# Optimization experiments

Hardware: AMD Instinct MI355X
Metric: run time of the kernel (lower is better)

Reference implementation:

```python
import jax, jax.numpy as jnp
import numpy as np

N_NODES = 100000
N_EDGES = 3200000
IN_CH = 128
HID = 32


def setup_inputs() -> dict:
    key = jax.random.key(0)
    k1, k2, k3, k4 = jax.random.split(key, 4)
    x = jax.random.normal(k1, (N_NODES, IN_CH), dtype=jnp.float32)
    edge_index = jax.random.randint(k2, (2, N_EDGES), 0, N_NODES, dtype=jnp.int64)
    # Glorot-style scale for weights
    W1 = jax.random.normal(k3, (IN_CH, HID), dtype=jnp.float32) * (1.0 / np.sqrt(IN_CH))
    b1 = jnp.zeros((HID,), dtype=jnp.float32)
    W2 = jax.random.normal(k4, (HID, HID), dtype=jnp.float32) * (1.0 / np.sqrt(HID))
    b2 = jnp.zeros((HID,), dtype=jnp.float32)
    return {"x": x, "edge_index": edge_index, "W1": W1, "b1": b1, "W2": W2, "b2": b2}


def _gcn_conv(x, src, dst, norm, W, b, n_nodes):
    # PyG GCNConv: h = x @ W, then symmetric-normalized scatter-add, then + bias
    h = x @ W                                   # [N, out]
    msg = h[src] * norm[:, None]                # gather + per-edge scale
    out = jax.ops.segment_sum(msg, dst, num_segments=n_nodes)  # scatter-add
    return out + b


def reference(x, edge_index, W1, b1, W2, b2):
    n = x.shape[0]
    loop = jnp.arange(n, dtype=edge_index.dtype)
    # add self-loops (PyG default add_self_loops=True)
    src = jnp.concatenate([edge_index[0], loop])
    dst = jnp.concatenate([edge_index[1], loop])
    # symmetric normalization deg^-1/2 on destination-side in-degree (incl. self-loops)
    deg = jax.ops.segment_sum(jnp.ones_like(dst, dtype=x.dtype), dst, num_segments=n)
    dinv = jnp.where(deg > 0, jax.lax.rsqrt(deg), 0.0)
    norm = dinv[src] * dinv[dst]                # [E + N]
    h = _gcn_conv(x, src, dst, norm, W1, b1, n)
    h = jax.nn.relu(h)
    out = _gcn_conv(h, src, dst, norm, W2, b2, n)
    return out
```

## Files before the change

kernel.cpp:

```cpp
#include <hip/hip_runtime.h>
#include <hip/hip_bf16.h>

#define N_NODES 100000
#define N_EDGES 3200000
#define IN_CH   128
#define HID     32
#define NB      1024
#define NPB     98
#define CAP     4096
#define CHUNK   4096
#define EPT     8
#define ACC_LD  33
#define NPASS   8
#define OCTN    12500u
#define FXS     1048576.0f
#define FXI     (1.0f/1048576.0f)
#define NTILE   6250
#define TPW     2

__device__ __forceinline__ unsigned int pack_bf16x2(float a, float b) {
    unsigned int ua = __float_as_uint(a);
    unsigned int ub = __float_as_uint(b);
    ua = (ua + 0x7FFFu + ((ua >> 16) & 1u)) >> 16;
    ub = (ub + 0x7FFFu + ((ub >> 16) & 1u)) >> 16;
    return (ua & 0xFFFFu) | (ub << 16);
}
__device__ __forceinline__ float bf_lo(unsigned int v) { return __uint_as_float(v << 16); }
__device__ __forceinline__ float bf_hi(unsigned int v) { return __uint_as_float(v & 0xFFFF0000u); }
__device__ __forceinline__ int   f2fx(float f)         { return (int)(f * FXS); }
__device__ __forceinline__ float hif(float f) {
    return __uint_as_float(__float_as_uint(f) & 0xFFFF0000u);
}
__device__ __forceinline__ unsigned int tpack(float a, float b) {
    return (__float_as_uint(a) >> 16) | (__float_as_uint(b) & 0xFFFF0000u);
}
__device__ __forceinline__ unsigned short bf16_rne(float f) {
    unsigned int u = __float_as_uint(f);
    return (unsigned short)((u + 0x7FFFu + ((u >> 16) & 1u)) >> 16);
}

typedef short bf16x8 __attribute__((ext_vector_type(8)));
typedef float f32x4  __attribute__((ext_vector_type(4)));
union frag_u { bf16x8 f; unsigned int u[4]; };

__global__ __launch_bounds__(256) void detect_idx(const int* __restrict__ ei,
                                                  int* __restrict__ flag) {
    __shared__ int nz;
    if (threadIdx.x == 0) nz = 0;
    __syncthreads();
    if (ei[2 * threadIdx.x + 1] != 0) atomicAdd(&nz, 1);
    __syncthreads();
    if (threadIdx.x == 0) flag[0] = (nz == 0) ? 1 : 0;
}

__device__ __forceinline__ int edge_at(const int* __restrict__ ei, int idx64,
                                       size_t pos) {
    if (idx64) return (int)((const long long*)ei)[pos];
    return ei[pos];
}

__global__ __launch_bounds__(256) void bcur_init(int* __restrict__ bcur) {
    int b = blockIdx.x * 256 + threadIdx.x;
    if (b < NB) bcur[b] = b * CAP;
}

__global__ __launch_bounds__(512) void bucket_scatter5(
    const int* __restrict__ ei,
    const int* __restrict__ flag,
    int* __restrict__ bcur,
    unsigned int* __restrict__ ebuf) {
    __shared__ int cnt[NB];
    __shared__ int loff[NB];
    __shared__ int dlt[NB];
    __shared__ int tmp[512];
    __shared__ unsigned int   sbuf[CHUNK];
    __shared__ unsigned short sbb[CHUNK];

    int t = threadIdx.x;
    for (int j = t; j < NB; j += 512) cnt[j] = 0;
    __syncthreads();

    int e0 = blockIdx.x * CHUNK;
    int nE = N_EDGES - e0; if (nE > CHUNK) nE = CHUNK;
    int idx64 = flag[0];

    unsigned int rs[EPT], rd[EPT];
#pragma unroll
    for (int j = 0; j < EPT; ++j) {
        int i = t + j * 512;
        if (i < nE) {
            rs[j] = (unsigned int)edge_at(ei, idx64, (size_t)(e0 + i));
            rd[j] = (unsigned int)edge_at(ei, idx64, (size_t)N_EDGES + e0 + i);
        }
    }

#pragma unroll
    for (int j = 0; j < EPT; ++j) {
        int i = t + j * 512;
        if (i < nE) atomicAdd(&cnt[rd[j] / NPB], 1);
    }
    __syncthreads();

    int c0 = cnt[2 * t], c1 = cnt[2 * t + 1];
    int s = c0 + c1;
    tmp[t] = s;
    __syncthreads();
    for (int off = 1; off < 512; off <<= 1) {
        int x = 0;
        if (t >= off) x = tmp[t - off];
        __syncthreads();
        if (t >= off) tmp[t] += x;
        __syncthreads();
    }
    int base = tmp[t] - s;
    loff[2 * t]     = base;
    loff[2 * t + 1] = base + c0;
    __syncthreads();

    for (int j = t; j < NB; j += 512) {
        int c = cnt[j];
        int gb = (c > 0) ? atomicAdd(&bcur[j], c) : 0;
        dlt[j] = gb - loff[j];
        cnt[j] = 0;
    }
    __syncthreads();

#pragma unroll
    for (int j = 0; j < EPT; ++j) {
        int i = t + j * 512;
        if (i < nE) {
            unsigned int b = rd[j] / NPB;
            int pos = loff[b] + atomicAdd(&cnt[b], 1);
            sbuf[pos] = (rs[j] << 8) | (rd[j] - b * NPB);
            sbb[pos]  = (unsigned short)b;
        }
    }
    __syncthreads();

    for (int i = t; i < nE; i += 512)
        ebuf[dlt[sbb[i]] + i] = sbuf[i];
}

__global__ __launch_bounds__(512) void finalize_csr(
    const int* __restrict__ bcur,
    unsigned int* __restrict__ ebuf,
    float* __restrict__ dinv,
    int* __restrict__ octp) {
    __shared__ unsigned int lbuf[CAP];
    __shared__ unsigned int sbuf[CAP];
    __shared__ int lhist[NPB];
    __shared__ int oh[8];
    __shared__ int obase[9];
    __shared__ int ocur[8];
    int b = blockIdx.x, t = threadIdx.x;
    int n0 = b * NPB;
    int nn = N_NODES - n0; if (nn > NPB) nn = NPB; if (nn < 0) nn = 0;
    int cnt = bcur[b] - b * CAP;
    unsigned int* reg = ebuf + (size_t)b * CAP;

    for (int j = t; j < NPB; j += 512) lhist[j] = 0;
    if (t < 8) oh[t] = 0;
    __syncthreads();

    for (int i = t; i < cnt; i += 512) {
        unsigned int e = reg[i];
        lbuf[i] = e;
        atomicAdd(&lhist[e & 255u], 1);
        atomicAdd(&oh[(e >> 8) / OCTN], 1);
    }
    __syncthreads();

    for (int j = t; j < nn; j += 512)
        dinv[n0 + j] = rsqrtf((float)(lhist[j] + 1));

    if (t == 0) {
        obase[0] = 0;
        for (int p = 0; p < 8; ++p) {
            obase[p + 1] = obase[p] + oh[p];
            ocur[p] = obase[p];
        }
    }
    __syncthreads();

    for (int i = t; i < cnt; i += 512) {
        unsigned int e = lbuf[i];
        int p = (int)((e >> 8) / OCTN);
        int pos = atomicAdd(&ocur[p], 1);
        sbuf[pos] = e;
    }
    __syncthreads();

    for (int i = t; i < cnt; i += 512)
        reg[i] = sbuf[i];
    if (t < 9) octp[b * 9 + t] = obase[t];
}

__global__ __launch_bounds__(256) void gemm1_mfma(
    const float* __restrict__ x,
    const float* __restrict__ W1,
    const float* __restrict__ dinv,
    unsigned short* __restrict__ h1u) {
    int wv   = blockIdx.x * 4 + (threadIdx.x >> 6);
    int lane = threadIdx.x & 63;
    int lq   = lane & 15;
    int kh   = lane >> 4;

    frag_u bh[2][4], bl[2][4];
#pragma unroll
    for (int t = 0; t < 2; ++t) {
#pragma unroll
        for (int s = 0; s < 4; ++s) {
            int ch = t * 16 + lq;
            int k0 = s * 32 + kh * 8;
            float w[8], wh[8];
#pragma unroll
            for (int i = 0; i < 8; ++i) {
                w[i]  = W1[(k0 + i) * HID + ch];
                wh[i] = hif(w[i]);
            }
#pragma unroll
            for (int j = 0; j < 4; ++j) {
                bh[t][s].u[j] = tpack(wh[2 * j], wh[2 * j + 1]);
                bl[t][s].u[j] = tpack(w[2 * j] - wh[2 * j],
                                      w[2 * j + 1] - wh[2 * j + 1]);
            }
        }
    }

#pragma unroll 1
    for (int it = 0; it < TPW; ++it) {
        int tile = wv * TPW + it;
        if (tile >= NTILE) return;
        int n0 = tile * 16;
        const float* xr = x + (size_t)(n0 + lq) * IN_CH;

        f32x4 acc0 = {0.f, 0.f, 0.f, 0.f};
        f32x4 acc1 = {0.f, 0.f, 0.f, 0.f};
#pragma unroll
        for (int s = 0; s < 4; ++s) {
            int k0 = s * 32 + kh * 8;
            float4 v0 = *reinterpret_cast<const float4*>(xr + k0);
            float4 v1 = *reinterpret_cast<const float4*>(xr + k0 + 4);
            frag_u ah, al;
            ah.u[0] = tpack(v0.x, v0.y);
            ah.u[1] = tpack(v0.z, v0.w);
            ah.u[2] = tpack(v1.x, v1.y);
            ah.u[3] = tpack(v1.z, v1.w);
            al.u[0] = tpack(v0.x - hif(v0.x), v0.y - hif(v0.y));
            al.u[1] = tpack(v0.z - hif(v0.z), v0.w - hif(v0.w));
            al.u[2] = tpack(v1.x - hif(v1.x), v1.y - hif(v1.y));
            al.u[3] = tpack(v1.z - hif(v1.z), v1.w - hif(v1.w));

            acc0 = __builtin_amdgcn_mfma_f32_16x16x32_bf16(ah.f, bh[0][s].f, acc0, 0, 0, 0);
            acc0 = __builtin_amdgcn_mfma_f32_16x16x32_bf16(al.f, bh[0][s].f, acc0, 0, 0, 0);
            acc0 = __builtin_amdgcn_mfma_f32_16x16x32_bf16(ah.f, bl[0][s].f, acc0, 0, 0, 0);
            acc1 = __builtin_amdgcn_mfma_f32_16x16x32_bf16(ah.f, bh[1][s].f, acc1, 0, 0, 0);
            acc1 = __builtin_amdgcn_mfma_f32_16x16x32_bf16(al.f, bh[1][s].f, acc1, 0, 0, 0);
            acc1 = __builtin_amdgcn_mfma_f32_16x16x32_bf16(ah.f, bl[1][s].f, acc1, 0, 0, 0);
        }

#pragma unroll
        for (int j = 0; j < 4; ++j) {
            int node = n0 + kh * 4 + j;
            float dn = dinv[node];
            unsigned short* dst = h1u + (size_t)node * 32 + lq;
            dst[0]  = bf16_rne(acc0[j] * dn);
            dst[16] = bf16_rne(acc1[j] * dn);
        }
    }
}

__device__ __forceinline__ uint4 row_q(const unsigned int* __restrict__ hb,
                                       unsigned int s, int q4) {
    return *reinterpret_cast<const uint4*>(hb + (size_t)s * 16 + q4);
}

__device__ __forceinline__ void fx_scatter8(int* acc, unsigned int e,
                                            int co, uint4 v) {
    int* a = acc + (int)(e & 255u) * ACC_LD + co;
    atomicAdd(&a[0], f2fx(bf_lo(v.x))); atomicAdd(&a[1], f2fx(bf_hi(v.x)));
    atomicAdd(&a[2], f2fx(bf_lo(v.y))); atomicAdd(&a[3], f2fx(bf_hi(v.y)));
    atomicAdd(&a[4], f2fx(bf_lo(v.z))); atomicAdd(&a[5], f2fx(bf_hi(v.z)));
    atomicAdd(&a[6], f2fx(bf_lo(v.w))); atomicAdd(&a[7], f2fx(bf_hi(v.w)));
}

__global__ __launch_bounds__(512, 8) void agg1_srt(
    const int* __restrict__ bcur,
    const unsigned int* __restrict__ ebuf,
    const int* __restrict__ octp,
    const unsigned int* __restrict__ h1b,
    const float* __restrict__ dinv,
    const float* __restrict__ b1,
    const float* __restrict__ W2,
    unsigned int* __restrict__ h3b) {
    __shared__ int acc[NPB * ACC_LD];
    __shared__ float w2s[HID * HID];
    __shared__ float b1s[HID];
    int b = blockIdx.x, t = threadIdx.x;
    int n0 = b * NPB;
    int nn = N_NODES - n0; if (nn > NPB) nn = NPB; if (nn < 0) nn = 0;
    const unsigned int* reg = ebuf + (size_t)b * CAP;

    for (int i = t; i < HID * HID; i += 512) w2s[i] = W2[i];
    if (t < HID) b1s[t] = b1[t];

    for (int u = t; u < nn * 4; u += 512) {
        int n = u >> 2, q = u & 3;
        uint4 sv = *reinterpret_cast<const uint4*>(h1b + (size_t)(n0 + n) * 16 + 4 * q);
        int* a = &acc[n * ACC_LD + 8 * q];
        a[0] = f2fx(bf_lo(sv.x)); a[1] = f2fx(bf_hi(sv.x));
        a[2] = f2fx(bf_lo(sv.y)); a[3] = f2fx(bf_hi(sv.y));
        a[4] = f2fx(bf_lo(sv.z)); a[5] = f2fx(bf_hi(sv.z));
        a[6] = f2fx(bf_lo(sv.w)); a[7] = f2fx(bf_hi(sv.w));
    }
    __syncthreads();

    int q4 = (t & 3) * 4;
    int co = (t & 3) * 8;
#pragma unroll 1
    for (int p = 0; p < NPASS; ++p) {
        int o1 = octp[b * 9 + p + 1];
        int i  = octp[b * 9 + p] + (t >> 2);
        for (; i + 128 < o1; i += 256) {
            unsigned int e0 = reg[i];
            unsigned int e1 = reg[i + 128];
            uint4 v0 = row_q(h1b, e0 >> 8, q4);
            uint4 v1 = row_q(h1b, e1 >> 8, q4);
            fx_scatter8(acc, e0, co, v0);
            fx_scatter8(acc, e1, co, v1);
        }
        if (i < o1) {
            unsigned int e = reg[i];
            uint4 v = row_q(h1b, e >> 8, q4);
            fx_scatter8(acc, e, co, v);
        }
    }
    __syncthreads();

    float* h2s = (float*)acc;
    for (int u = t; u < nn * HID; u += 512) {
        int n = u >> 5, j = u & 31;
        float v = (float)acc[n * ACC_LD + j] * FXI * dinv[n0 + n] + b1s[j];
        h2s[n * ACC_LD + j] = v > 0.f ? v : 0.f;
    }
    __syncthreads();

    for (int u = t; u < nn * 4; u += 512) {
        int n = u >> 2, qq = u & 3;
        const float* h2 = &h2s[n * ACC_LD];
        float a2[8];
#pragma unroll
        for (int k = 0; k < 8; ++k) a2[k] = 0.f;
#pragma unroll
        for (int j = 0; j < HID; ++j) {
            float hj = h2[j];
            const float* wr = &w2s[j * HID + 8 * qq];
#pragma unroll
            for (int k = 0; k < 8; ++k) a2[k] += hj * wr[k];
        }
        float dn = dinv[n0 + n];
        unsigned int* dst = h3b + (size_t)(n0 + n) * 16 + 4 * qq;
        *reinterpret_cast<uint4*>(dst) = make_uint4(
            pack_bf16x2(a2[0] * dn, a2[1] * dn),
            pack_bf16x2(a2[2] * dn, a2[3] * dn),
            pack_bf16x2(a2[4] * dn, a2[5] * dn),
            pack_bf16x2(a2[6] * dn, a2[7] * dn));
    }
}

__global__ __launch_bounds__(512, 8) void agg2_srt(
    const int* __restrict__ bcur,
    const unsigned int* __restrict__ ebuf,
    const int* __restrict__ octp,
    const unsigned int* __restrict__ h3b,
    const float* __restrict__ dinv,
    const float* __restrict__ b2,
    float* __restrict__ out) {
    __shared__ int acc[NPB * ACC_LD];
    __shared__ float b2s[HID];
    int b = blockIdx.x, t = threadIdx.x;
    int n0 = b * NPB;
    int nn = N_NODES - n0; if (nn > NPB) nn = NPB; if (nn < 0) nn = 0;
    const unsigned int* reg = ebuf + (size_t)b * CAP;

    if (t < HID) b2s[t] = b2[t];

    for (int u = t; u < nn * 4; u += 512) {
        int n = u >> 2, q = u & 3;
        uint4 sv = *reinterpret_cast<const uint4*>(h3b + (size_t)(n0 + n) * 16 + 4 * q);
        int* a = &acc[n * ACC_LD + 8 * q];
        a[0] = f2fx(bf_lo(sv.x)); a[1] = f2fx(bf_hi(sv.x));
        a[2] = f2fx(bf_lo(sv.y)); a[3] = f2fx(bf_hi(sv.y));
        a[4] = f2fx(bf_lo(sv.z)); a[5] = f2fx(bf_hi(sv.z));
        a[6] = f2fx(bf_lo(sv.w)); a[7] = f2fx(bf_hi(sv.w));
    }
    __syncthreads();

    int q4 = (t & 3) * 4;
    int co = (t & 3) * 8;
#pragma unroll 1
    for (int p = 0; p < NPASS; ++p) {
        int o1 = octp[b * 9 + p + 1];
        int i  = octp[b * 9 + p] + (t >> 2);
        for (; i + 128 < o1; i += 256) {
            unsigned int e0 = reg[i];
            unsigned int e1 = reg[i + 128];
            uint4 v0 = row_q(h3b, e0 >> 8, q4);
            uint4 v1 = row_q(h3b, e1 >> 8, q4);
            fx_scatter8(acc, e0, co, v0);
            fx_scatter8(acc, e1, co, v1);
        }
        if (i < o1) {
            unsigned int e = reg[i];
            uint4 v = row_q(h3b, e >> 8, q4);
            fx_scatter8(acc, e, co, v);
        }
    }
    __syncthreads();

    for (int u = t; u < nn * 4; u += 512) {
        int n = u >> 2, qq = u & 3;
        float dn = dinv[n0 + n];
        const int* a = &acc[n * ACC_LD + 8 * qq];
        const float* bb = &b2s[8 * qq];
        float4 o1v, o2v;
        o1v.x = (float)a[0] * FXI * dn + bb[0];
        o1v.y = (float)a[1] * FXI * dn + bb[1];
        o1v.z = (float)a[2] * FXI * dn + bb[2];
        o1v.w = (float)a[3] * FXI * dn + bb[3];
        o2v.x = (float)a[4] * FXI * dn + bb[4];
        o2v.y = (float)a[5] * FXI * dn + bb[5];
        o2v.z = (float)a[6] * FXI * dn + bb[6];
        o2v.w = (float)a[7] * FXI * dn + bb[7];
        float* op = out + (size_t)(n0 + n) * 32 + 8 * qq;
        *reinterpret_cast<float4*>(op)     = o1v;
        *reinterpret_cast<float4*>(op + 4) = o2v;
    }
}

extern "C" void kernel_launch(void* const* d_in, const int* in_sizes, int n_in,
                              void* d_out, int out_size, void* d_ws, size_t ws_size,
                              hipStream_t stream) {
    const float* x  = (const float*)d_in[0];
    const int*   ei = (const int*)d_in[1];
    const float* W1 = (const float*)d_in[2];
    const float* b1 = (const float*)d_in[3];
    const float* W2 = (const float*)d_in[4];
    const float* b2 = (const float*)d_in[5];
    float* out = (float*)d_out;

    int*          flag = (int*)d_ws;
    int*          bcur = flag + 64;
    int*          octp = bcur + NB;
    float*        dinv = (float*)(octp + NB * 9);
    unsigned int* ebuf = (unsigned int*)(dinv + N_NODES);
    unsigned int* h1b  = ebuf + (size_t)NB * CAP;
    unsigned int* h3b  = h1b + (size_t)N_NODES * 16;

    const int chunkBlocks = (N_EDGES + CHUNK - 1) / CHUNK;
    const int g1Blocks    = (NTILE + 4 * TPW - 1) / (4 * TPW);

    detect_idx<<<1, 256, 0, stream>>>(ei, flag);

    bcur_init<<<(NB + 255) / 256, 256, 0, stream>>>(bcur);
    bucket_scatter5<<<chunkBlocks, 512, 0, stream>>>(ei, flag, bcur, ebuf);
    finalize_csr<<<NB, 512, 0, stream>>>(bcur, ebuf, dinv, octp);

    gemm1_mfma<<<g1Blocks, 256, 0, stream>>>(x, W1, dinv,
                                             (unsigned short*)h1b);
    agg1_srt<<<NB, 512, 0, stream>>>(bcur, ebuf, octp, h1b, dinv, b1, W2, h3b);

    agg2_srt<<<NB, 512, 0, stream>>>(bcur, ebuf, octp, h3b, dinv, b2, out);
}
```

Baseline: 218.3 us.

## Flatten aggregation loops, merge init kernels, enlarge scatter chunks, rotate bucket atomics

Several changes at once. The aggregation kernels drop the per-octant pass structure and octp table and walk each bucket's edges in one flat loop unrolled by four. bcur initialization is folded into the detect kernel, which removes one launch. The bucket scatter doubles its chunk size and edges per thread and rotates the order of its global atomics per block to spread contention. finalize_csr moves to 256 threads. It still sorts edges by source octant, so locality is kept while the per-pass loop overhead goes away; the larger scatter chunks raise LDS use and lower the block count.

```diff
diff --git a/kernel.cpp b/kernel.cpp
--- a/kernel.cpp
+++ b/kernel.cpp
@@ -8,10 +8,9 @@
 #define NB      1024
 #define NPB     98
 #define CAP     4096
-#define CHUNK   4096
-#define EPT     8
+#define CHUNK   8192
+#define EPT     16
 #define ACC_LD  33
-#define NPASS   8
 #define OCTN    12500u
 #define FXS     1048576.0f
 #define FXI     (1.0f/1048576.0f)
@@ -43,9 +42,11 @@
 typedef float f32x4  __attribute__((ext_vector_type(4)));
 union frag_u { bf16x8 f; unsigned int u[4]; };
 
-__global__ __launch_bounds__(256) void detect_idx(const int* __restrict__ ei,
-                                                  int* __restrict__ flag) {
+__global__ __launch_bounds__(256) void detect_init(const int* __restrict__ ei,
+                                                   int* __restrict__ flag,
+                                                   int* __restrict__ bcur) {
     __shared__ int nz;
+    for (int j = threadIdx.x; j < NB; j += 256) bcur[j] = j * CAP;
     if (threadIdx.x == 0) nz = 0;
     __syncthreads();
     if (ei[2 * threadIdx.x + 1] != 0) atomicAdd(&nz, 1);
@@ -59,12 +60,7 @@
     return ei[pos];
 }
 
-__global__ __launch_bounds__(256) void bcur_init(int* __restrict__ bcur) {
-    int b = blockIdx.x * 256 + threadIdx.x;
-    if (b < NB) bcur[b] = b * CAP;
-}
-
-__global__ __launch_bounds__(512) void bucket_scatter5(
+__global__ __launch_bounds__(512) void scatter7(
     const int* __restrict__ ei,
     const int* __restrict__ flag,
     int* __restrict__ bcur,
@@ -117,7 +113,9 @@
     loff[2 * t + 1] = base + c0;
     __syncthreads();
 
-    for (int j = t; j < NB; j += 512) {
+    int rot = (blockIdx.x * 211) & (NB - 1);
+    for (int jj = t; jj < NB; jj += 512) {
+        int j = (jj + rot) & (NB - 1);
         int c = cnt[j];
         int gb = (c > 0) ? atomicAdd(&bcur[j], c) : 0;
         dlt[j] = gb - loff[j];
@@ -141,16 +139,15 @@
         ebuf[dlt[sbb[i]] + i] = sbuf[i];
 }
 
-__global__ __launch_bounds__(512) void finalize_csr(
+__global__ __launch_bounds__(256) void finalize_csr(
     const int* __restrict__ bcur,
     unsigned int* __restrict__ ebuf,
-    float* __restrict__ dinv,
-    int* __restrict__ octp) {
+    float* __restrict__ dinv) {
     __shared__ unsigned int lbuf[CAP];
     __shared__ unsigned int sbuf[CAP];
     __shared__ int lhist[NPB];
     __shared__ int oh[8];
-    __shared__ int obase[9];
+    __shared__ int obase[8];
     __shared__ int ocur[8];
     int b = blockIdx.x, t = threadIdx.x;
     int n0 = b * NPB;
@@ -158,11 +155,11 @@
     int cnt = bcur[b] - b * CAP;
     unsigned int* reg = ebuf + (size_t)b * CAP;
 
-    for (int j = t; j < NPB; j += 512) lhist[j] = 0;
+    for (int j = t; j < NPB; j += 256) lhist[j] = 0;
     if (t < 8) oh[t] = 0;
     __syncthreads();
 
-    for (int i = t; i < cnt; i += 512) {
+    for (int i = t; i < cnt; i += 256) {
         unsigned int e = reg[i];
         lbuf[i] = e;
         atomicAdd(&lhist[e & 255u], 1);
@@ -170,19 +167,18 @@
     }
     __syncthreads();
 
-    for (int j = t; j < nn; j += 512)
+    for (int j = t; j < nn; j += 256)
         dinv[n0 + j] = rsqrtf((float)(lhist[j] + 1));
 
     if (t == 0) {
-        obase[0] = 0;
+        int run = 0;
         for (int p = 0; p < 8; ++p) {
-            obase[p + 1] = obase[p] + oh[p];
-            ocur[p] = obase[p];
-        }
-    }
-    __syncthreads();
-
-    for (int i = t; i < cnt; i += 512) {
+            obase[p] = run; ocur[p] = run; run += oh[p];
+        }
+    }
+    __syncthreads();
+
+    for (int i = t; i < cnt; i += 256) {
         unsigned int e = lbuf[i];
         int p = (int)((e >> 8) / OCTN);
         int pos = atomicAdd(&ocur[p], 1);
@@ -190,9 +186,8 @@
     }
     __syncthreads();
 
-    for (int i = t; i < cnt; i += 512)
+    for (int i = t; i < cnt; i += 256)
         reg[i] = sbuf[i];
-    if (t < 9) octp[b * 9 + t] = obase[t];
 }
 
 __global__ __launch_bounds__(256) void gemm1_mfma(
@@ -284,10 +279,9 @@
     atomicAdd(&a[6], f2fx(bf_lo(v.w))); atomicAdd(&a[7], f2fx(bf_hi(v.w)));
 }
 
-__global__ __launch_bounds__(512, 8) void agg1_srt(
+__global__ __launch_bounds__(512, 8) void agg1_flat(
     const int* __restrict__ bcur,
     const unsigned int* __restrict__ ebuf,
-    const int* __restrict__ octp,
     const unsigned int* __restrict__ h1b,
     const float* __restrict__ dinv,
     const float* __restrict__ b1,
@@ -299,6 +293,7 @@
     int b = blockIdx.x, t = threadIdx.x;
     int n0 = b * NPB;
     int nn = N_NODES - n0; if (nn > NPB) nn = NPB; if (nn < 0) nn = 0;
+    int cnt = bcur[b] - b * CAP;
     const unsigned int* reg = ebuf + (size_t)b * CAP;
 
     for (int i = t; i < HID * HID; i += 512) w2s[i] = W2[i];
@@ -317,23 +312,25 @@
 
     int q4 = (t & 3) * 4;
     int co = (t & 3) * 8;
-#pragma unroll 1
-    for (int p = 0; p < NPASS; ++p) {
-        int o1 = octp[b * 9 + p + 1];
-        int i  = octp[b * 9 + p] + (t >> 2);
-        for (; i + 128 < o1; i += 256) {
-            unsigned int e0 = reg[i];
-            unsigned int e1 = reg[i + 128];
-            uint4 v0 = row_q(h1b, e0 >> 8, q4);
-            uint4 v1 = row_q(h1b, e1 >> 8, q4);
-            fx_scatter8(acc, e0, co, v0);
-            fx_scatter8(acc, e1, co, v1);
-        }
-        if (i < o1) {
-            unsigned int e = reg[i];
-            uint4 v = row_q(h1b, e >> 8, q4);
-            fx_scatter8(acc, e, co, v);
-        }
+    int i  = t >> 2;
+    for (; i + 384 < cnt; i += 512) {
+        unsigned int e0 = reg[i];
+        unsigned int e1 = reg[i + 128];
+        unsigned int e2 = reg[i + 256];
+        unsigned int e3 = reg[i + 384];
+        uint4 v0 = row_q(h1b, e0 >> 8, q4);
+        uint4 v1 = row_q(h1b, e1 >> 8, q4);
+        uint4 v2 = row_q(h1b, e2 >> 8, q4);
+        uint4 v3 = row_q(h1b, e3 >> 8, q4);
+        fx_scatter8(acc, e0, co, v0);
+        fx_scatter8(acc, e1, co, v1);
+        fx_scatter8(acc, e2, co, v2);
+        fx_scatter8(acc, e3, co, v3);
+    }
+    for (; i < cnt; i += 128) {
+        unsigned int e = reg[i];
+        uint4 v = row_q(h1b, e >> 8, q4);
+        fx_scatter8(acc, e, co, v);
     }
     __syncthreads();
 
@@ -368,10 +365,9 @@
     }
 }
 
-__global__ __launch_bounds__(512, 8) void agg2_srt(
+__global__ __launch_bounds__(512, 8) void agg2_flat(
     const int* __restrict__ bcur,
     const unsigned int* __restrict__ ebuf,
-    const int* __restrict__ octp,
     const unsigned int* __restrict__ h3b,
     const float* __restrict__ dinv,
     const float* __restrict__ b2,
@@ -381,6 +377,7 @@
     int b = blockIdx.x, t = threadIdx.x;
     int n0 = b * NPB;
     int nn = N_NODES - n0; if (nn > NPB) nn = NPB; if (nn < 0) nn = 0;
+    int cnt = bcur[b] - b * CAP;
     const unsigned int* reg = ebuf + (size_t)b * CAP;
 
     if (t < HID) b2s[t] = b2[t];
@@ -398,23 +395,25 @@
 
     int q4 = (t & 3) * 4;
     int co = (t & 3) * 8;
-#pragma unroll 1
-    for (int p = 0; p < NPASS; ++p) {
-        int o1 = octp[b * 9 + p + 1];
-        int i  = octp[b * 9 + p] + (t >> 2);
-        for (; i + 128 < o1; i += 256) {
-            unsigned int e0 = reg[i];
-            unsigned int e1 = reg[i + 128];
-            uint4 v0 = row_q(h3b, e0 >> 8, q4);
-            uint4 v1 = row_q(h3b, e1 >> 8, q4);
-            fx_scatter8(acc, e0, co, v0);
-            fx_scatter8(acc, e1, co, v1);
-        }
-        if (i < o1) {
-            unsigned int e = reg[i];
-            uint4 v = row_q(h3b, e >> 8, q4);
-            fx_scatter8(acc, e, co, v);
-        }
+    int i  = t >> 2;
+    for (; i + 384 < cnt; i += 512) {
+        unsigned int e0 = reg[i];
+        unsigned int e1 = reg[i + 128];
+        unsigned int e2 = reg[i + 256];
+        unsigned int e3 = reg[i + 384];
+        uint4 v0 = row_q(h3b, e0 >> 8, q4);
+        uint4 v1 = row_q(h3b, e1 >> 8, q4);
+        uint4 v2 = row_q(h3b, e2 >> 8, q4);
+        uint4 v3 = row_q(h3b, e3 >> 8, q4);
+        fx_scatter8(acc, e0, co, v0);
+        fx_scatter8(acc, e1, co, v1);
+        fx_scatter8(acc, e2, co, v2);
+        fx_scatter8(acc, e3, co, v3);
+    }
+    for (; i < cnt; i += 128) {
+        unsigned int e = reg[i];
+        uint4 v = row_q(h3b, e >> 8, q4);
+        fx_scatter8(acc, e, co, v);
     }
     __syncthreads();
 
@@ -451,8 +450,7 @@
 
     int*          flag = (int*)d_ws;
     int*          bcur = flag + 64;
-    int*          octp = bcur + NB;
-    float*        dinv = (float*)(octp + NB * 9);
+    float*        dinv = (float*)(bcur + NB);
     unsigned int* ebuf = (unsigned int*)(dinv + N_NODES);
     unsigned int* h1b  = ebuf + (size_t)NB * CAP;
     unsigned int* h3b  = h1b + (size_t)N_NODES * 16;
@@ -460,15 +458,14 @@
     const int chunkBlocks = (N_EDGES + CHUNK - 1) / CHUNK;
     const int g1Blocks    = (NTILE + 4 * TPW - 1) / (4 * TPW);
 
-    detect_idx<<<1, 256, 0, stream>>>(ei, flag);
-
-    bcur_init<<<(NB + 255) / 256, 256, 0, stream>>>(bcur);
-    bucket_scatter5<<<chunkBlocks, 512, 0, stream>>>(ei, flag, bcur, ebuf);
-    finalize_csr<<<NB, 512, 0, stream>>>(bcur, ebuf, dinv, octp);
+    detect_init<<<1, 256, 0, stream>>>(ei, flag, bcur);
+
+    scatter7<<<chunkBlocks, 512, 0, stream>>>(ei, flag, bcur, ebuf);
+    finalize_csr<<<NB, 256, 0, stream>>>(bcur, ebuf, dinv);
 
     gemm1_mfma<<<g1Blocks, 256, 0, stream>>>(x, W1, dinv,
                                              (unsigned short*)h1b);
-    agg1_srt<<<NB, 512, 0, stream>>>(bcur, ebuf, octp, h1b, dinv, b1, W2, h3b);
-
-    agg2_srt<<<NB, 512, 0, stream>>>(bcur, ebuf, octp, h3b, dinv, b2, out);
-}
+    agg1_flat<<<NB, 512, 0, stream>>>(bcur, ebuf, h1b, dinv, b1, W2, h3b);
+
+    agg2_flat<<<NB, 512, 0, stream>>>(bcur, ebuf, h3b, dinv, b2, out);
+}
```

New measurement: 203.0 us. 7.0% less time.
